# Kernel tuning notes

Measured on AMD Instinct MI355X. Metric: run time of the kernel, lower is better.

The kernel has to match this reference:

```python
import jax, jax.numpy as jnp
import numpy as np

B, F, S, H = 8, 512, 8192, 8
D = F // H
GROUPS = F // 16  # GroupNorm group_cnt = channels // 16
EPS = 1e-8


def group_norm(x, gamma, beta):
    # x: [B, C, S]; normalize per (group-channels, spatial) like torch GroupNorm
    b, c, s = x.shape
    xg = x.reshape(b, GROUPS, c // GROUPS, s)
    mu = xg.mean(axis=(2, 3), keepdims=True)
    var = xg.var(axis=(2, 3), keepdims=True)
    xn = ((xg - mu) * jax.lax.rsqrt(var + EPS)).reshape(b, c, s)
    return xn * gamma[None, :, None] + beta[None, :, None]


def setup_inputs() -> dict:
    key = jax.random.key(0)
    ks = jax.random.split(key, 5)
    return {
        "hidden_states": jax.random.normal(ks[0], (B, F, S), jnp.float32),
        "qkv_w": jax.random.normal(ks[1], (3, H, D, F), jnp.float32) * 0.02,
        "qkv_b": jnp.zeros((3, 1, 1, H, D), jnp.float32),
        "out_proj": jax.random.normal(ks[2], (F, F), jnp.float32) * 0.02,
        "gn1_gamma": jnp.ones((F,), jnp.float32),
        "gn1_beta": jnp.zeros((F,), jnp.float32),
        "gn2_gamma": jnp.ones((F,), jnp.float32),
        "gn2_beta": jnp.zeros((F,), jnp.float32),
        # torch init is zeros; use small random so the gated branch is exercised
        "gate_g": jax.random.normal(ks[3], (F, 1), jnp.float32) * 0.1,
    }


def reference(hidden_states, qkv_w, qkv_b, out_proj,
              gn1_gamma, gn1_beta, gn2_gamma, gn2_beta, gate_g):
    x = group_norm(hidden_states, gn1_gamma, gn1_beta)
    # [3, B, S, H, D]
    qkv = jnp.einsum('bfl,ihdf->iblhd', x, qkv_w) + qkv_b
    q = jax.nn.elu(qkv[0]) + 1.0
    k = jax.nn.elu(qkv[1]) + 1.0
    v = qkv[2]
    # global non-causal linear attention: KV = sum_l k_l v_l^T  -> [B,H,D,D]
    kv = jnp.einsum('blhf,blhF->bhFf', k, v)
    k_sum = jnp.sum(k, axis=1, keepdims=True)               # [B,1,H,D]
    z = jnp.sum(q * k_sum, axis=-1, keepdims=True)          # [B,S,H,1]
    qz = q / z
    out = jnp.einsum('blhf,bhFf->blhF', qz, kv)             # [B,S,H,D]
    out = out.reshape(out.shape[0], out.shape[1], -1)       # [B,S,F]
    y = jnp.einsum('blf,Ff->bFl', out, out_proj)            # [B,F,S]
    y = group_norm(y, gn2_gamma, gn2_beta)
    # rezero-style gate: residual + per-channel gate * branch
    return hidden_states + gate_g[None] * y
```

## Files before the change

### kernel.cpp

```cpp
#include <hip/hip_runtime.h>
#include <hip/hip_bf16.h>

#define BB 8
#define FF 512
#define SS 8192
#define HH 8
#define DD 64
#define N1 1536

typedef __hip_bfloat16 bf16;
typedef __attribute__((ext_vector_type(8))) short bf16x8;
typedef __attribute__((ext_vector_type(4))) float f32x4;

__device__ __forceinline__ float us2f(unsigned short u) {
    union { unsigned int i; float f; } x; x.i = ((unsigned int)u) << 16; return x.f;
}
__device__ __forceinline__ unsigned short f2b(float f) {
    unsigned int u = __builtin_bit_cast(unsigned int, f);
    return (unsigned short)((u + 0x7FFFu + ((u >> 16) & 1u)) >> 16);
}
__device__ __forceinline__ void gll16(const void* g, void* l) {
    __builtin_amdgcn_global_load_lds((const __attribute__((address_space(1))) void*)g,
                                     (__attribute__((address_space(3))) void*)l, 16, 0, 0);
}
__device__ __forceinline__ bf16x8 fragld(const unsigned short* base, int row, int quad) {
    int off = row * 32 + (((quad + (row >> 1)) & 3) << 3);
    return *(const bf16x8*)(base + off);
}

__global__ void gn1_part(const float* __restrict__ hid, float* __restrict__ part) {
    int bg = blockIdx.x;
    const float4* base = (const float4*)(hid + ((size_t)(bg >> 5) * FF + (bg & 31) * 16) * SS);
    float s = 0.f, s2 = 0.f;
    int t0 = blockIdx.y * 4096 + threadIdx.x;
    #pragma unroll
    for (int it = 0; it < 16; it++) {
        float4 x = base[t0 + it * 256];
        s  += x.x + x.y + x.z + x.w;
        s2 += x.x * x.x + x.y * x.y + x.z * x.z + x.w * x.w;
    }
    #pragma unroll
    for (int off = 32; off > 0; off >>= 1) {
        s  += __shfl_down(s, off, 64);
        s2 += __shfl_down(s2, off, 64);
    }
    __shared__ float rs_[8];
    int wid = threadIdx.x >> 6, lane = threadIdx.x & 63;
    if (lane == 0) { rs_[wid] = s; rs_[wid + 4] = s2; }
    __syncthreads();
    if (threadIdx.x == 0)
        atomicAdd(&part[bg * 2], rs_[0] + rs_[1] + rs_[2] + rs_[3]);
    else if (threadIdx.x == 64)
        atomicAdd(&part[bg * 2 + 1], rs_[4] + rs_[5] + rs_[6] + rs_[7]);
}

__global__ void gn_final(const float* __restrict__ part, const float* __restrict__ gamma,
                         const float* __restrict__ beta, const float* __restrict__ gate,
                         float* __restrict__ sc, float* __restrict__ sh) {
    int c = blockIdx.x * 256 + threadIdx.x;
    int ch = c & 511;
    int bg = (c >> 9) * 32 + (ch >> 4);
    float ts = part[bg * 2], ts2 = part[bg * 2 + 1];
    float mu  = ts * (1.f / 131072.f);
    float var = ts2 * (1.f / 131072.f) - mu * mu;
    float r   = rsqrtf(var + 1e-8f);
    float scv = gamma[ch] * r;
    float shv = beta[ch] - mu * scv;
    if (gate) { float gv = gate[ch]; scv *= gv; shv *= gv; }
    sc[c] = scv; sh[c] = shv;
}

__global__ void gn_final2(const float* __restrict__ part2, const float* __restrict__ gamma,
                          const float* __restrict__ beta, const float* __restrict__ gate,
                          float* __restrict__ sc, float* __restrict__ sh) {
    int c = blockIdx.x * 256 + threadIdx.x;
    int ch = c & 511;
    int bg = ((c >> 9) << 5) + (ch >> 4);
    const float2* pp = (const float2*)part2 + ((size_t)bg << 7);
    float ts = 0.f, ts2 = 0.f;
    #pragma unroll 8
    for (int i = 0; i < 128; i++) { float2 v = pp[i]; ts += v.x; ts2 += v.y; }
    float mu  = ts * (1.f / 131072.f);
    float var = ts2 * (1.f / 131072.f) - mu * mu;
    float r   = rsqrtf(var + 1e-8f);
    float gv  = gate[ch];
    float scv = gamma[ch] * r;
    sc[c] = gv * scv;
    sh[c] = gv * (beta[ch] - mu * scv);
}

__global__ void castb(const float* __restrict__ s, unsigned short* __restrict__ d, int n4) {
    int i = blockIdx.x * 256 + threadIdx.x;
    if (i >= n4) return;
    float4 v = ((const float4*)s)[i];
    ushort4 u = make_ushort4(f2b(v.x), f2b(v.y), f2b(v.z), f2b(v.w));
    ((ushort4*)d)[i] = u;
}

__global__ void xn_prep(const float* __restrict__ hid, const float* __restrict__ sc,
                        const float* __restrict__ sh, unsigned short* __restrict__ xnA) {
    int b = blockIdx.z, f0 = blockIdx.y * 64, l0 = blockIdx.x * 64;
    __shared__ float t[64][65];
    int tid = threadIdx.x;
    #pragma unroll
    for (int it = 0; it < 16; it++) {
        int idx = it * 256 + tid;
        int f = idx >> 6, l = idx & 63;
        int fg = f0 + f;
        t[f][l] = hid[((size_t)b * FF + fg) * SS + l0 + l] * sc[b * FF + fg] + sh[b * FF + fg];
    }
    __syncthreads();
    #pragma unroll
    for (int it = 0; it < 4; it++) {
        int idx = it * 256 + tid;
        int l = idx >> 4, fq = (idx & 15) * 4;
        ushort4 u = make_ushort4(f2b(t[fq + 0][l]), f2b(t[fq + 1][l]),
                                 f2b(t[fq + 2][l]), f2b(t[fq + 3][l]));
        *(ushort4*)(xnA + ((size_t)b * SS + l0 + l) * FF + f0 + fq) = u;
    }
}

template<int KV>
__global__ __launch_bounds__(256) void gemm1_mfma(
    const unsigned short* __restrict__ A, const unsigned short* __restrict__ Bw,
    const float* __restrict__ bias,
    unsigned short* __restrict__ q, unsigned short* __restrict__ kT,
    unsigned short* __restrict__ vT) {
    __shared__ unsigned short smem[16384] __attribute__((aligned(16)));
    unsigned short* As = smem;
    unsigned short* Bs = smem + 4096;
    const int b = blockIdx.z;
    const int m0 = blockIdx.x * 128;
    const int n0 = (KV ? 512 : 0) + blockIdx.y * 128;
    const int tid = threadIdx.x;
    const int w = tid >> 6, ln = tid & 63;
    const int wr = w >> 1, wc = w & 1;
    const int lrow = ln & 15, quad = ln >> 4;

    const int ch0 = tid, ch1 = tid + 256;
    const int ra = ch0 >> 2, ca = ((ch0 & 3) - (ra >> 1)) & 3;
    const int rb = ch1 >> 2, cb = ((ch1 & 3) - (rb >> 1)) & 3;
    const unsigned short* pA0 = A + ((size_t)b * SS + m0 + ra) * FF + ca * 8;
    const unsigned short* pA1 = A + ((size_t)b * SS + m0 + rb) * FF + cb * 8;
    const unsigned short* pB0 = Bw + (size_t)(n0 + ra) * FF + ca * 8;
    const unsigned short* pB1 = Bw + (size_t)(n0 + rb) * FF + cb * 8;
    unsigned short* lA0 = As + ch0 * 8; unsigned short* lA1 = As + ch1 * 8;
    unsigned short* lB0 = Bs + ch0 * 8; unsigned short* lB1 = Bs + ch1 * 8;

    f32x4 acc[4][4];
    #pragma unroll
    for (int j = 0; j < 4; j++)
        #pragma unroll
        for (int i = 0; i < 4; i++) acc[j][i] = (f32x4){0.f, 0.f, 0.f, 0.f};

    for (int kk = 0; kk < 16; kk++) {
        gll16(pA0, lA0); gll16(pA1, lA1); gll16(pB0, lB0); gll16(pB1, lB1);
        pA0 += 32; pA1 += 32; pB0 += 32; pB1 += 32;
        __syncthreads();
        bf16x8 af[4], bm[4];
        #pragma unroll
        for (int j = 0; j < 4; j++) af[j] = fragld(Bs, wc * 64 + j * 16 + lrow, quad);
        #pragma unroll
        for (int i = 0; i < 4; i++) bm[i] = fragld(As, wr * 64 + i * 16 + lrow, quad);
        if constexpr (KV == 0) {
            #pragma unroll
            for (int j = 0; j < 4; j++)
                #pragma unroll
                for (int i = 0; i < 4; i++)
                    acc[j][i] = __builtin_amdgcn_mfma_f32_16x16x32_bf16(af[j], bm[i], acc[j][i], 0, 0, 0);
        } else {
            #pragma unroll
            for (int i = 0; i < 4; i++)
                #pragma unroll
                for (int j = 0; j < 4; j++)
                    acc[i][j] = __builtin_amdgcn_mfma_f32_16x16x32_bf16(bm[i], af[j], acc[i][j], 0, 0, 0);
        }
        __syncthreads();
    }

    const int cc = tid & 15, rr = tid >> 4;
    if constexpr (KV == 0) {
        const int n0v = n0 + (wc << 6);
        const int cni = (wc << 3) + (quad >> 1);
        const int ni4 = (quad & 1) << 2;
        #pragma unroll
        for (int j = 0; j < 4; j++) {
            const float* bp = bias + n0v + (j << 4) + (quad << 2);
            float b0 = bp[0], b1 = bp[1], b2 = bp[2], b3 = bp[3];
            #pragma unroll
            for (int i = 0; i < 4; i++) {
                float v0 = acc[j][i][0] + b0, v1 = acc[j][i][1] + b1;
                float v2 = acc[j][i][2] + b2, v3 = acc[j][i][3] + b3;
                v0 = v0 > 0.f ? v0 + 1.f : __expf(v0);
                v1 = v1 > 0.f ? v1 + 1.f : __expf(v1);
                v2 = v2 > 0.f ? v2 + 1.f : __expf(v2);
                v3 = v3 > 0.f ? v3 + 1.f : __expf(v3);
                int ml = (wr << 6) + (i << 4) + lrow;
                int chk = (cni + (j << 1)) ^ (ml & 7);
                *(ushort4*)(smem + ml * 128 + (chk << 3) + ni4) =
                    make_ushort4(f2b(v0), f2b(v1), f2b(v2), f2b(v3));
            }
        }
        __syncthreads();
        const size_t brow = (size_t)b * SS + m0;
        #pragma unroll
        for (int p = 0; p < 8; p++) {
            int ml = (p << 4) + rr;
            bf16x8 vv = *(const bf16x8*)(smem + ml * 128 + ((cc ^ (ml & 7)) << 3));
            *(bf16x8*)(q + (brow + ml) * FF + n0 + (cc << 3)) = vv;
        }
    } else {
        const bool isk = (n0 < 1024);
        unsigned short* outp = isk ? kT : vT;
        const int cmi = (wr << 3) + (quad >> 1);
        const int mi4 = (quad & 1) << 2;
        #pragma unroll
        for (int j = 0; j < 4; j++) {
            const int nl = (wc << 6) + (j << 4) + lrow;
            const float bv = bias[n0 + nl];
            #pragma unroll
            for (int i = 0; i < 4; i++) {
                float v0 = acc[i][j][0] + bv, v1 = acc[i][j][1] + bv;
                float v2 = acc[i][j][2] + bv, v3 = acc[i][j][3] + bv;
                if (isk) {
                    v0 = v0 > 0.f ? v0 + 1.f : __expf(v0);
                    v1 = v1 > 0.f ? v1 + 1.f : __expf(v1);
                    v2 = v2 > 0.f ? v2 + 1.f : __expf(v2);
                    v3 = v3 > 0.f ? v3 + 1.f : __expf(v3);
                }
                int chk = (cmi + (i << 1)) ^ (nl & 7);
                *(ushort4*)(smem + nl * 128 + (chk << 3) + mi4) =
                    make_ushort4(f2b(v0), f2b(v1), f2b(v2), f2b(v3));
            }
        }
        __syncthreads();
        const int nb = n0 & 511;
        #pragma unroll
        for (int p = 0; p < 8; p++) {
            int nl = (p << 4) + rr;
            bf16x8 vv = *(const bf16x8*)(smem + nl * 128 + ((cc ^ (nl & 7)) << 3));
            int nq = nb + nl;
            *(bf16x8*)(outp + (((size_t)b * HH + (nq >> 6)) * DD + (nq & 63)) * SS
                       + m0 + (cc << 3)) = vv;
        }
    }
}

__global__ __launch_bounds__(256) void kv_mfma(
    const unsigned short* __restrict__ kT, const unsigned short* __restrict__ vT,
    float* __restrict__ kv, float* __restrict__ kpart) {
    const int bh = blockIdx.x;
    const int l0 = blockIdx.y * 512;
    const int tid = threadIdx.x;

    {
        int f = tid >> 2, part = tid & 3;
        const unsigned short* kp = kT + ((size_t)bh * DD + f) * SS + l0 + part * 128;
        float s = 0.f;
        #pragma unroll
        for (int c = 0; c < 16; c++) {
            bf16x8 u = *(const bf16x8*)(kp + c * 8);
            #pragma unroll
            for (int j = 0; j < 8; j++) s += us2f((unsigned short)u[j]);
        }
        s += __shfl_down(s, 1, 64);
        s += __shfl_down(s, 2, 64);
        if (part == 0) kpart[(size_t)bh * 1024 + blockIdx.y * 64 + f] = s;
    }

    const int w = tid >> 6, ln = tid & 63;
    const int lrow = ln & 15, quad = ln >> 4;
    f32x4 acc[4];
    #pragma unroll
    for (int ft = 0; ft < 4; ft++) acc[ft] = (f32x4){0.f, 0.f, 0.f, 0.f};
    const unsigned short* vbase = vT + ((size_t)bh * DD + w * 16 + lrow) * SS + l0;
    const unsigned short* kbase = kT + ((size_t)bh * DD + lrow) * SS + l0;
    for (int ks = 0; ks < 16; ks++) {
        bf16x8 vf = *(const bf16x8*)(vbase + ks * 32 + quad * 8);
        #pragma unroll
        for (int ft = 0; ft < 4; ft++) {
            bf16x8 kf = *(const bf16x8*)(kbase + (size_t)(ft * 16) * SS + ks * 32 + quad * 8);
            acc[ft] = __builtin_amdgcn_mfma_f32_16x16x32_bf16(vf, kf, acc[ft], 0, 0, 0);
        }
    }
    float* kvp = kv + (size_t)bh * 4096;
    #pragma unroll
    for (int ft = 0; ft < 4; ft++) {
        #pragma unroll
        for (int r = 0; r < 4; r++) {
            int e = w * 16 + (quad << 2) + r;
            int f = ft * 16 + lrow;
            atomicAdd(&kvp[e * 64 + f], acc[ft][r]);
        }
    }
}

__global__ void kvcast(const float* __restrict__ kv, unsigned short* __restrict__ kv16,
                       const float* __restrict__ kpart, float* __restrict__ ksm) {
    int i = blockIdx.x * 256 + threadIdx.x;
    float4 v = ((const float4*)kv)[i];
    ((ushort4*)kv16)[i] = make_ushort4(f2b(v.x), f2b(v.y), f2b(v.z), f2b(v.w));
    if (i < 4096) {
        const float* kp = kpart + ((size_t)(i >> 6)) * 1024 + (i & 63);
        float s = 0.f;
        #pragma unroll
        for (int c = 0; c < 16; c++) s += kp[c * 64];
        ksm[i] = s;
    }
}

__global__ __launch_bounds__(256) void attn_mfma(
    const unsigned short* __restrict__ q, const unsigned short* __restrict__ kv16,
    const float* __restrict__ ksum, unsigned short* __restrict__ attn) {
    const int bh = blockIdx.y, b = bh >> 3, h = bh & 7;
    const int l0 = blockIdx.x * 128;
    __shared__ float ksS[64];
    __shared__ float zS[128];
    const int tid = threadIdx.x;
    if (tid < 64) ksS[tid] = ksum[bh * DD + tid];
    __syncthreads();
    if (tid < 128) {
        const unsigned short* qp = q + ((size_t)b * SS + l0 + tid) * FF + h * DD;
        float z = 0.f;
        #pragma unroll
        for (int c = 0; c < 8; c++) {
            bf16x8 u = *(const bf16x8*)(qp + c * 8);
            #pragma unroll
            for (int j = 0; j < 8; j++) z += us2f((unsigned short)u[j]) * ksS[c * 8 + j];
        }
        zS[tid] = 1.f / z;
    }
    __syncthreads();

    const int w = tid >> 6, ln = tid & 63;
    const int lrow = ln & 15, quad = ln >> 4;
    const unsigned short* kvp = kv16 + (size_t)bh * 4096;
    bf16x8 kvf[4][2];
    #pragma unroll
    for (int et = 0; et < 4; et++)
        #pragma unroll
        for (int ks = 0; ks < 2; ks++)
            kvf[et][ks] = *(const bf16x8*)(kvp + (et * 16 + lrow) * 64 + ks * 32 + quad * 8);

    f32x4 acc[2][4];
    #pragma unroll
    for (int lt = 0; lt < 2; lt++)
        #pragma unroll
        for (int et = 0; et < 4; et++) acc[lt][et] = (f32x4){0.f, 0.f, 0.f, 0.f};

    const unsigned short* qbase = q + ((size_t)b * SS + l0 + w * 32) * FF + h * DD;
    #pragma unroll
    for (int lt = 0; lt < 2; lt++) {
        #pragma unroll
        for (int ks = 0; ks < 2; ks++) {
            bf16x8 qf = *(const bf16x8*)(qbase + (size_t)(lt * 16 + lrow) * FF + ks * 32 + quad * 8);
            #pragma unroll
            for (int et = 0; et < 4; et++)
                acc[lt][et] = __builtin_amdgcn_mfma_f32_16x16x32_bf16(kvf[et][ks], qf, acc[lt][et], 0, 0, 0);
        }
    }
    #pragma unroll
    for (int lt = 0; lt < 2; lt++) {
        int lloc = w * 32 + lt * 16 + lrow;
        float zi = zS[lloc];
        unsigned short* op = attn + ((size_t)b * SS + l0 + lloc) * FF + h * DD;
        #pragma unroll
        for (int et = 0; et < 4; et++) {
            ushort4 u = make_ushort4(f2b(acc[lt][et][0] * zi), f2b(acc[lt][et][1] * zi),
                                     f2b(acc[lt][et][2] * zi), f2b(acc[lt][et][3] * zi));
            *(ushort4*)(op + et * 16 + (quad << 2)) = u;
        }
    }
}

__global__ __launch_bounds__(256) void gemm2_mfma(
    const unsigned short* __restrict__ A, const unsigned short* __restrict__ Bw,
    unsigned short* __restrict__ y, float* __restrict__ gpart2) {
    __shared__ unsigned short smem[16384] __attribute__((aligned(16)));
    unsigned short* As = smem;
    unsigned short* Bs = smem + 4096;
    const int b = blockIdx.z;
    const int m0 = blockIdx.x * 128, n0 = blockIdx.y * 128;
    const int tid = threadIdx.x;
    const int w = tid >> 6, ln = tid & 63;
    const int wr = w >> 1, wc = w & 1;
    const int lrow = ln & 15, quad = ln >> 4;

    const int ch0 = tid, ch1 = tid + 256;
    const int ra = ch0 >> 2, ca = ((ch0 & 3) - (ra >> 1)) & 3;
    const int rb = ch1 >> 2, cb = ((ch1 & 3) - (rb >> 1)) & 3;
    const unsigned short* pA0 = A + ((size_t)b * SS + m0 + ra) * FF + ca * 8;
    const unsigned short* pA1 = A + ((size_t)b * SS + m0 + rb) * FF + cb * 8;
    const unsigned short* pB0 = Bw + (size_t)(n0 + ra) * FF + ca * 8;
    const unsigned short* pB1 = Bw + (size_t)(n0 + rb) * FF + cb * 8;
    unsigned short* lA0 = As + ch0 * 8; unsigned short* lA1 = As + ch1 * 8;
    unsigned short* lB0 = Bs + ch0 * 8; unsigned short* lB1 = Bs + ch1 * 8;

    f32x4 acc[4][4];
    #pragma unroll
    for (int i = 0; i < 4; i++)
        #pragma unroll
        for (int j = 0; j < 4; j++) acc[i][j] = (f32x4){0.f, 0.f, 0.f, 0.f};

    for (int kk = 0; kk < 16; kk++) {
        gll16(pA0, lA0); gll16(pA1, lA1); gll16(pB0, lB0); gll16(pB1, lB1);
        pA0 += 32; pA1 += 32; pB0 += 32; pB1 += 32;
        __syncthreads();
        bf16x8 am[4], bn[4];
        #pragma unroll
        for (int i = 0; i < 4; i++) am[i] = fragld(As, wr * 64 + i * 16 + lrow, quad);
        #pragma unroll
        for (int j = 0; j < 4; j++) bn[j] = fragld(Bs, wc * 64 + j * 16 + lrow, quad);
        #pragma unroll
        for (int i = 0; i < 4; i++)
            #pragma unroll
            for (int j = 0; j < 4; j++)
                acc[i][j] = __builtin_amdgcn_mfma_f32_16x16x32_bf16(am[i], bn[j], acc[i][j], 0, 0, 0);
        __syncthreads();
    }
    const int cmi = (wr << 3) + (quad >> 1);
    const int mi4 = (quad & 1) << 2;
    #pragma unroll
    for (int j = 0; j < 4; j++) {
        const int nl = (wc << 6) + (j << 4) + lrow;
        float sj = 0.f, s2j = 0.f;
        #pragma unroll
        for (int i = 0; i < 4; i++) {
            float v0 = acc[i][j][0], v1 = acc[i][j][1], v2 = acc[i][j][2], v3 = acc[i][j][3];
            sj  += v0 + v1 + v2 + v3;
            s2j += v0 * v0 + v1 * v1 + v2 * v2 + v3 * v3;
            int chk = (cmi + (i << 1)) ^ (nl & 7);
            *(ushort4*)(smem + nl * 128 + (chk << 3) + mi4) =
                make_ushort4(f2b(v0), f2b(v1), f2b(v2), f2b(v3));
        }
        #pragma unroll
        for (int off = 32; off > 0; off >>= 1) {
            sj  += __shfl_down(sj, off, 64);
            s2j += __shfl_down(s2j, off, 64);
        }
        if (ln == 0) {
            int g = (n0 >> 4) + (wc << 2) + j;
            size_t slot = ((((size_t)b << 5) + g) << 7) + (blockIdx.x << 1) + wr;
            gpart2[slot * 2]     = sj;
            gpart2[slot * 2 + 1] = s2j;
        }
    }
    __syncthreads();
    const int cc = tid & 15, rr = tid >> 4;
    #pragma unroll
    for (int p = 0; p < 8; p++) {
        int nl = (p << 4) + rr;
        bf16x8 vv = *(const bf16x8*)(smem + nl * 128 + ((cc ^ (nl & 7)) << 3));
        *(bf16x8*)(y + ((size_t)b * FF + n0 + nl) * SS + m0 + (cc << 3)) = vv;
    }
}

__global__ void final_kernel(const float* __restrict__ hid, const bf16* __restrict__ y,
                             const float* __restrict__ gsc, const float* __restrict__ gsh,
                             float* __restrict__ out) {
    int bf = blockIdx.x;
    float a = gsc[bf], c0 = gsh[bf];
    const float4*  hp = (const float4*)(hid + (size_t)bf * SS);
    const ushort4* yp = (const ushort4*)(y + (size_t)bf * SS);
    float4* op = (float4*)(out + (size_t)bf * SS);
    for (int t = threadIdx.x; t < 2048; t += 256) {
        float4 hv = hp[t];
        ushort4 yv = yp[t];
        float4 r;
        r.x = hv.x + a * us2f(yv.x) + c0;
        r.y = hv.y + a * us2f(yv.y) + c0;
        r.z = hv.z + a * us2f(yv.z) + c0;
        r.w = hv.w + a * us2f(yv.w) + c0;
        op[t] = r;
    }
}

extern "C" void kernel_launch(void* const* d_in, const int* in_sizes, int n_in,
                              void* d_out, int out_size, void* d_ws, size_t ws_size,
                              hipStream_t stream) {
    const float* hid      = (const float*)d_in[0];
    const float* qkv_w    = (const float*)d_in[1];
    const float* qkv_b    = (const float*)d_in[2];
    const float* out_proj = (const float*)d_in[3];
    const float* g1       = (const float*)d_in[4];
    const float* b1       = (const float*)d_in[5];
    const float* g2       = (const float*)d_in[6];
    const float* b2       = (const float*)d_in[7];
    const float* gate     = (const float*)d_in[8];
    float* out = (float*)d_out;

    char* p = (char*)d_ws;
    float* sc1 = (float*)p; p += (size_t)4096 * 4;
    float* sh1 = (float*)p; p += (size_t)4096 * 4;
    float* gsc = (float*)p; p += (size_t)4096 * 4;
    float* gsh = (float*)p; p += (size_t)4096 * 4;
    float* kvb = (float*)p; p += (size_t)262144 * 4;
    float* ksm = (float*)p; p += (size_t)4096 * 4;
    float* gnp = (float*)p; p += (size_t)1024 * 4;
    unsigned short* kv16 = (unsigned short*)p; p += (size_t)262144 * 2;
    unsigned short* Wb = (unsigned short*)p; p += (size_t)786432 * 2;
    unsigned short* Pb = (unsigned short*)p; p += (size_t)262144 * 2;
    unsigned short* qb = (unsigned short*)p; p += (size_t)33554432 * 2;
    unsigned short* kTb = (unsigned short*)p; p += (size_t)33554432 * 2;
    unsigned short* vTb = (unsigned short*)p;
    unsigned short* attn = kTb;
    unsigned short* yb   = vTb;
    unsigned short* xnA  = (unsigned short*)d_out;
    float* kpart  = (float*)((char*)d_out + (size_t)64 * 1024 * 1024);
    float* gpart2 = (float*)((char*)d_out + (size_t)64 * 1024 * 1024 + 262144);

    hipMemsetAsync(kvb, 0, (size_t)(262144 + 4096 + 1024) * 4, stream);

    gn1_part<<<dim3(256, 8), 256, 0, stream>>>(hid, gnp);
    gn_final<<<16, 256, 0, stream>>>(gnp, g1, b1, nullptr, sc1, sh1);
    castb<<<768, 256, 0, stream>>>(qkv_w, Wb, 196608);
    castb<<<256, 256, 0, stream>>>(out_proj, Pb, 65536);
    xn_prep<<<dim3(128, 8, 8), 256, 0, stream>>>(hid, sc1, sh1, xnA);
    gemm1_mfma<0><<<dim3(64, 4, 8), 256, 0, stream>>>(xnA, Wb, qkv_b, qb, kTb, vTb);
    gemm1_mfma<1><<<dim3(64, 8, 8), 256, 0, stream>>>(xnA, Wb, qkv_b, qb, kTb, vTb);
    kv_mfma<<<dim3(64, 16), 256, 0, stream>>>(kTb, vTb, kvb, kpart);
    kvcast<<<256, 256, 0, stream>>>(kvb, kv16, kpart, ksm);
    attn_mfma<<<dim3(64, 64), 256, 0, stream>>>(qb, kv16, ksm, attn);
    gemm2_mfma<<<dim3(64, 4, 8), 256, 0, stream>>>(attn, Pb, yb, gpart2);
    gn_final2<<<16, 256, 0, stream>>>(gpart2, g2, b2, gate, gsc, gsh);
    final_kernel<<<4096, 256, 0, stream>>>(hid, (const bf16*)yb, gsc, gsh, out);
}
```

Measured before the change: 623.8 us.

## Fuse K/V projection GEMM with KV outer-product reduction per head tile

The K/V projection GEMM now tiles by head, so each block computes K and V for one head and a 128-row slice of the sequence. The block then builds the partial K^T V product and the K column sums straight from shared memory, adding them into kv with atomics. This removes writing the kT/vT intermediates to global memory, reading them back, and the separate kv_mfma launch. In exchange the atomic traffic grows, since there are now 64 sequence chunks per head instead of 16, and kvcast must reduce 64 partial sums per column.

```diff
diff --git a/kernel.cpp b/kernel.cpp
--- a/kernel.cpp
+++ b/kernel.cpp
@@ -120,18 +120,15 @@
     }
 }
 
-template<int KV>
-__global__ __launch_bounds__(256) void gemm1_mfma(
+__global__ __launch_bounds__(256) void gemm1_q(
     const unsigned short* __restrict__ A, const unsigned short* __restrict__ Bw,
-    const float* __restrict__ bias,
-    unsigned short* __restrict__ q, unsigned short* __restrict__ kT,
-    unsigned short* __restrict__ vT) {
+    const float* __restrict__ bias, unsigned short* __restrict__ q) {
     __shared__ unsigned short smem[16384] __attribute__((aligned(16)));
     unsigned short* As = smem;
     unsigned short* Bs = smem + 4096;
     const int b = blockIdx.z;
     const int m0 = blockIdx.x * 128;
-    const int n0 = (KV ? 512 : 0) + blockIdx.y * 128;
+    const int n0 = blockIdx.y * 128;
     const int tid = threadIdx.x;
     const int w = tid >> 6, ln = tid & 63;
     const int wr = w >> 1, wc = w & 1;
@@ -162,135 +159,159 @@
         for (int j = 0; j < 4; j++) af[j] = fragld(Bs, wc * 64 + j * 16 + lrow, quad);
         #pragma unroll
         for (int i = 0; i < 4; i++) bm[i] = fragld(As, wr * 64 + i * 16 + lrow, quad);
-        if constexpr (KV == 0) {
+        #pragma unroll
+        for (int j = 0; j < 4; j++)
+            #pragma unroll
+            for (int i = 0; i < 4; i++)
+                acc[j][i] = __builtin_amdgcn_mfma_f32_16x16x32_bf16(af[j], bm[i], acc[j][i], 0, 0, 0);
+        __syncthreads();
+    }
+
+    const int cc = tid & 15, rr = tid >> 4;
+    const int n0v = n0 + (wc << 6);
+    const int cni = (wc << 3) + (quad >> 1);
+    const int ni4 = (quad & 1) << 2;
+    #pragma unroll
+    for (int j = 0; j < 4; j++) {
+        const float* bp = bias + n0v + (j << 4) + (quad << 2);
+        float b0 = bp[0], b1 = bp[1], b2 = bp[2], b3 = bp[3];
+        #pragma unroll
+        for (int i = 0; i < 4; i++) {
+            float v0 = acc[j][i][0] + b0, v1 = acc[j][i][1] + b1;
+            float v2 = acc[j][i][2] + b2, v3 = acc[j][i][3] + b3;
+            v0 = v0 > 0.f ? v0 + 1.f : __expf(v0);
+            v1 = v1 > 0.f ? v1 + 1.f : __expf(v1);
+            v2 = v2 > 0.f ? v2 + 1.f : __expf(v2);
+            v3 = v3 > 0.f ? v3 + 1.f : __expf(v3);
+            int ml = (wr << 6) + (i << 4) + lrow;
+            int chk = (cni + (j << 1)) ^ (ml & 7);
+            *(ushort4*)(smem + ml * 128 + (chk << 3) + ni4) =
+                make_ushort4(f2b(v0), f2b(v1), f2b(v2), f2b(v3));
+        }
+    }
+    __syncthreads();
+    const size_t brow = (size_t)b * SS + m0;
+    #pragma unroll
+    for (int p = 0; p < 8; p++) {
+        int ml = (p << 4) + rr;
+        bf16x8 vv = *(const bf16x8*)(smem + ml * 128 + ((cc ^ (ml & 7)) << 3));
+        *(bf16x8*)(q + (brow + ml) * FF + n0 + (cc << 3)) = vv;
+    }
+}
+
+__global__ __launch_bounds__(256) void gemm1_kv(
+    const unsigned short* __restrict__ A, const unsigned short* __restrict__ Bw,
+    const float* __restrict__ bias,
+    float* __restrict__ kv, float* __restrict__ kpart) {
+    __shared__ unsigned short smem[16384] __attribute__((aligned(16)));
+    unsigned short* As = smem;
+    unsigned short* Bs = smem + 4096;
+    const int b = blockIdx.z;
+    const int h = blockIdx.y;
+    const int m0 = blockIdx.x * 128;
+    const int tid = threadIdx.x;
+    const int w = tid >> 6, ln = tid & 63;
+    const int wr = w >> 1, wc = w & 1;
+    const int lrow = ln & 15, quad = ln >> 4;
+
+    const int ch0 = tid, ch1 = tid + 256;
+    const int ra = ch0 >> 2, ca = ((ch0 & 3) - (ra >> 1)) & 3;
+    const int rb = ch1 >> 2, cb = ((ch1 & 3) - (rb >> 1)) & 3;
+    const int bra = 512 + ((ra >> 6) << 9) + (h << 6) + (ra & 63);
+    const int brb = 512 + ((rb >> 6) << 9) + (h << 6) + (rb & 63);
+    const unsigned short* pA0 = A + ((size_t)b * SS + m0 + ra) * FF + ca * 8;
+    const unsigned short* pA1 = A + ((size_t)b * SS + m0 + rb) * FF + cb * 8;
+    const unsigned short* pB0 = Bw + (size_t)bra * FF + ca * 8;
+    const unsigned short* pB1 = Bw + (size_t)brb * FF + cb * 8;
+    unsigned short* lA0 = As + ch0 * 8; unsigned short* lA1 = As + ch1 * 8;
+    unsigned short* lB0 = Bs + ch0 * 8; unsigned short* lB1 = Bs + ch1 * 8;
+
+    f32x4 acc[4][4];
+    #pragma unroll
+    for (int i = 0; i < 4; i++)
+        #pragma unroll
+        for (int j = 0; j < 4; j++) acc[i][j] = (f32x4){0.f, 0.f, 0.f, 0.f};
+
+    for (int kk = 0; kk < 16; kk++) {
+        gll16(pA0, lA0); gll16(pA1, lA1); gll16(pB0, lB0); gll16(pB1, lB1);
+        pA0 += 32; pA1 += 32; pB0 += 32; pB1 += 32;
+        __syncthreads();
+        bf16x8 af[4], bm[4];
+        #pragma unroll
+        for (int j = 0; j < 4; j++) af[j] = fragld(Bs, wc * 64 + j * 16 + lrow, quad);
+        #pragma unroll
+        for (int i = 0; i < 4; i++) bm[i] = fragld(As, wr * 64 + i * 16 + lrow, quad);
+        #pragma unroll
+        for (int i = 0; i < 4; i++)
             #pragma unroll
             for (int j = 0; j < 4; j++)
-                #pragma unroll
-                for (int i = 0; i < 4; i++)
-                    acc[j][i] = __builtin_amdgcn_mfma_f32_16x16x32_bf16(af[j], bm[i], acc[j][i], 0, 0, 0);
-        } else {
-            #pragma unroll
-            for (int i = 0; i < 4; i++)
-                #pragma unroll
-                for (int j = 0; j < 4; j++)
-                    acc[i][j] = __builtin_amdgcn_mfma_f32_16x16x32_bf16(bm[i], af[j], acc[i][j], 0, 0, 0);
-        }
+                acc[i][j] = __builtin_amdgcn_mfma_f32_16x16x32_bf16(bm[i], af[j], acc[i][j], 0, 0, 0);
         __syncthreads();
     }
 
-    const int cc = tid & 15, rr = tid >> 4;
-    if constexpr (KV == 0) {
-        const int n0v = n0 + (wc << 6);
-        const int cni = (wc << 3) + (quad >> 1);
-        const int ni4 = (quad & 1) << 2;
-        #pragma unroll
-        for (int j = 0; j < 4; j++) {
-            const float* bp = bias + n0v + (j << 4) + (quad << 2);
-            float b0 = bp[0], b1 = bp[1], b2 = bp[2], b3 = bp[3];
-            #pragma unroll
-            for (int i = 0; i < 4; i++) {
-                float v0 = acc[j][i][0] + b0, v1 = acc[j][i][1] + b1;
-                float v2 = acc[j][i][2] + b2, v3 = acc[j][i][3] + b3;
+    const bool isk = (wc == 0);
+    const int cmi = (wr << 3) + (quad >> 1);
+    const int mi4 = (quad & 1) << 2;
+    #pragma unroll
+    for (int j = 0; j < 4; j++) {
+        const int nl = (wc << 6) + (j << 4) + lrow;
+        const int nabs = 512 + ((nl >> 6) << 9) + (h << 6) + (nl & 63);
+        const float bv = bias[nabs];
+        #pragma unroll
+        for (int i = 0; i < 4; i++) {
+            float v0 = acc[i][j][0] + bv, v1 = acc[i][j][1] + bv;
+            float v2 = acc[i][j][2] + bv, v3 = acc[i][j][3] + bv;
+            if (isk) {
                 v0 = v0 > 0.f ? v0 + 1.f : __expf(v0);
                 v1 = v1 > 0.f ? v1 + 1.f : __expf(v1);
                 v2 = v2 > 0.f ? v2 + 1.f : __expf(v2);
                 v3 = v3 > 0.f ? v3 + 1.f : __expf(v3);
-                int ml = (wr << 6) + (i << 4) + lrow;
-                int chk = (cni + (j << 1)) ^ (ml & 7);
-                *(ushort4*)(smem + ml * 128 + (chk << 3) + ni4) =
-                    make_ushort4(f2b(v0), f2b(v1), f2b(v2), f2b(v3));
             }
-        }
-        __syncthreads();
-        const size_t brow = (size_t)b * SS + m0;
-        #pragma unroll
-        for (int p = 0; p < 8; p++) {
-            int ml = (p << 4) + rr;
-            bf16x8 vv = *(const bf16x8*)(smem + ml * 128 + ((cc ^ (ml & 7)) << 3));
-            *(bf16x8*)(q + (brow + ml) * FF + n0 + (cc << 3)) = vv;
-        }
-    } else {
-        const bool isk = (n0 < 1024);
-        unsigned short* outp = isk ? kT : vT;
-        const int cmi = (wr << 3) + (quad >> 1);
-        const int mi4 = (quad & 1) << 2;
-        #pragma unroll
-        for (int j = 0; j < 4; j++) {
-            const int nl = (wc << 6) + (j << 4) + lrow;
-            const float bv = bias[n0 + nl];
-            #pragma unroll
-            for (int i = 0; i < 4; i++) {
-                float v0 = acc[i][j][0] + bv, v1 = acc[i][j][1] + bv;
-                float v2 = acc[i][j][2] + bv, v3 = acc[i][j][3] + bv;
-                if (isk) {
-                    v0 = v0 > 0.f ? v0 + 1.f : __expf(v0);
-                    v1 = v1 > 0.f ? v1 + 1.f : __expf(v1);
-                    v2 = v2 > 0.f ? v2 + 1.f : __expf(v2);
-                    v3 = v3 > 0.f ? v3 + 1.f : __expf(v3);
-                }
-                int chk = (cmi + (i << 1)) ^ (nl & 7);
-                *(ushort4*)(smem + nl * 128 + (chk << 3) + mi4) =
-                    make_ushort4(f2b(v0), f2b(v1), f2b(v2), f2b(v3));
-            }
-        }
-        __syncthreads();
-        const int nb = n0 & 511;
-        #pragma unroll
-        for (int p = 0; p < 8; p++) {
-            int nl = (p << 4) + rr;
-            bf16x8 vv = *(const bf16x8*)(smem + nl * 128 + ((cc ^ (nl & 7)) << 3));
-            int nq = nb + nl;
-            *(bf16x8*)(outp + (((size_t)b * HH + (nq >> 6)) * DD + (nq & 63)) * SS
-                       + m0 + (cc << 3)) = vv;
-        }
-    }
-}
-
-__global__ __launch_bounds__(256) void kv_mfma(
-    const unsigned short* __restrict__ kT, const unsigned short* __restrict__ vT,
-    float* __restrict__ kv, float* __restrict__ kpart) {
-    const int bh = blockIdx.x;
-    const int l0 = blockIdx.y * 512;
-    const int tid = threadIdx.x;
+            int chk = (cmi + (i << 1)) ^ (nl & 7);
+            *(ushort4*)(smem + nl * 128 + (chk << 3) + mi4) =
+                make_ushort4(f2b(v0), f2b(v1), f2b(v2), f2b(v3));
+        }
+    }
+    __syncthreads();
 
     {
         int f = tid >> 2, part = tid & 3;
-        const unsigned short* kp = kT + ((size_t)bh * DD + f) * SS + l0 + part * 128;
         float s = 0.f;
         #pragma unroll
-        for (int c = 0; c < 16; c++) {
-            bf16x8 u = *(const bf16x8*)(kp + c * 8);
+        for (int c = 0; c < 4; c++) {
+            int chk = ((part << 2) + c) ^ (f & 7);
+            bf16x8 u = *(const bf16x8*)(smem + f * 128 + (chk << 3));
             #pragma unroll
-            for (int j = 0; j < 8; j++) s += us2f((unsigned short)u[j]);
+            for (int jj = 0; jj < 8; jj++) s += us2f((unsigned short)u[jj]);
         }
         s += __shfl_down(s, 1, 64);
         s += __shfl_down(s, 2, 64);
-        if (part == 0) kpart[(size_t)bh * 1024 + blockIdx.y * 64 + f] = s;
-    }
-
-    const int w = tid >> 6, ln = tid & 63;
-    const int lrow = ln & 15, quad = ln >> 4;
-    f32x4 acc[4];
-    #pragma unroll
-    for (int ft = 0; ft < 4; ft++) acc[ft] = (f32x4){0.f, 0.f, 0.f, 0.f};
-    const unsigned short* vbase = vT + ((size_t)bh * DD + w * 16 + lrow) * SS + l0;
-    const unsigned short* kbase = kT + ((size_t)bh * DD + lrow) * SS + l0;
-    for (int ks = 0; ks < 16; ks++) {
-        bf16x8 vf = *(const bf16x8*)(vbase + ks * 32 + quad * 8);
+        if (part == 0)
+            kpart[(((size_t)(b * HH + h)) * 64 + blockIdx.x) * 64 + f] = s;
+    }
+
+    f32x4 kacc[4];
+    #pragma unroll
+    for (int ft = 0; ft < 4; ft++) kacc[ft] = (f32x4){0.f, 0.f, 0.f, 0.f};
+    const int vrow = 64 + (w << 4) + lrow;
+    #pragma unroll
+    for (int ks = 0; ks < 4; ks++) {
+        bf16x8 vf = *(const bf16x8*)(smem + vrow * 128 + ((((ks << 2) + quad) ^ (vrow & 7)) << 3));
         #pragma unroll
         for (int ft = 0; ft < 4; ft++) {
-            bf16x8 kf = *(const bf16x8*)(kbase + (size_t)(ft * 16) * SS + ks * 32 + quad * 8);
-            acc[ft] = __builtin_amdgcn_mfma_f32_16x16x32_bf16(vf, kf, acc[ft], 0, 0, 0);
-        }
-    }
-    float* kvp = kv + (size_t)bh * 4096;
+            int krow = (ft << 4) + lrow;
+            bf16x8 kf = *(const bf16x8*)(smem + krow * 128 + ((((ks << 2) + quad) ^ (krow & 7)) << 3));
+            kacc[ft] = __builtin_amdgcn_mfma_f32_16x16x32_bf16(vf, kf, kacc[ft], 0, 0, 0);
+        }
+    }
+    float* kvp = kv + (size_t)(b * HH + h) * 4096;
     #pragma unroll
     for (int ft = 0; ft < 4; ft++) {
         #pragma unroll
         for (int r = 0; r < 4; r++) {
-            int e = w * 16 + (quad << 2) + r;
-            int f = ft * 16 + lrow;
-            atomicAdd(&kvp[e * 64 + f], acc[ft][r]);
+            int e = (w << 4) + (quad << 2) + r;
+            int f = (ft << 4) + lrow;
+            atomicAdd(&kvp[e * 64 + f], kacc[ft][r]);
         }
     }
 }
@@ -301,10 +322,10 @@
     float4 v = ((const float4*)kv)[i];
     ((ushort4*)kv16)[i] = make_ushort4(f2b(v.x), f2b(v.y), f2b(v.z), f2b(v.w));
     if (i < 4096) {
-        const float* kp = kpart + ((size_t)(i >> 6)) * 1024 + (i & 63);
+        const float* kp = kpart + ((size_t)(i >> 6)) * 4096 + (i & 63);
         float s = 0.f;
-        #pragma unroll
-        for (int c = 0; c < 16; c++) s += kp[c * 64];
+        #pragma unroll 8
+        for (int c = 0; c < 64; c++) s += kp[c * 64];
         ksm[i] = s;
     }
 }
@@ -501,13 +522,11 @@
     unsigned short* Wb = (unsigned short*)p; p += (size_t)786432 * 2;
     unsigned short* Pb = (unsigned short*)p; p += (size_t)262144 * 2;
     unsigned short* qb = (unsigned short*)p; p += (size_t)33554432 * 2;
-    unsigned short* kTb = (unsigned short*)p; p += (size_t)33554432 * 2;
-    unsigned short* vTb = (unsigned short*)p;
-    unsigned short* attn = kTb;
-    unsigned short* yb   = vTb;
+    unsigned short* attn = (unsigned short*)p; p += (size_t)33554432 * 2;
+    unsigned short* yb   = (unsigned short*)p;
     unsigned short* xnA  = (unsigned short*)d_out;
     float* kpart  = (float*)((char*)d_out + (size_t)64 * 1024 * 1024);
-    float* gpart2 = (float*)((char*)d_out + (size_t)64 * 1024 * 1024 + 262144);
+    float* gpart2 = (float*)((char*)d_out + (size_t)64 * 1024 * 1024 + 1048576);
 
     hipMemsetAsync(kvb, 0, (size_t)(262144 + 4096 + 1024) * 4, stream);
 
@@ -516,9 +535,8 @@
     castb<<<768, 256, 0, stream>>>(qkv_w, Wb, 196608);
     castb<<<256, 256, 0, stream>>>(out_proj, Pb, 65536);
     xn_prep<<<dim3(128, 8, 8), 256, 0, stream>>>(hid, sc1, sh1, xnA);
-    gemm1_mfma<0><<<dim3(64, 4, 8), 256, 0, stream>>>(xnA, Wb, qkv_b, qb, kTb, vTb);
-    gemm1_mfma<1><<<dim3(64, 8, 8), 256, 0, stream>>>(xnA, Wb, qkv_b, qb, kTb, vTb);
-    kv_mfma<<<dim3(64, 16), 256, 0, stream>>>(kTb, vTb, kvb, kpart);
+    gemm1_q<<<dim3(64, 4, 8), 256, 0, stream>>>(xnA, Wb, qkv_b, qb);
+    gemm1_kv<<<dim3(64, 8, 8), 256, 0, stream>>>(xnA, Wb, qkv_b, kvb, kpart);
     kvcast<<<256, 256, 0, stream>>>(kvb, kv16, kpart, ksm);
     attn_mfma<<<dim3(64, 64), 256, 0, stream>>>(qb, kv16, ksm, attn);
     gemm2_mfma<<<dim3(64, 4, 8), 256, 0, stream>>>(attn, Pb, yb, gpart2);
```

After: 609.9 us. -2.2%, faster.
